# Performance work log

Hardware: AMD Instinct MI355X
Metric: run time of the kernel (lower is better)

Reference implementation:

```python
import jax, jax.numpy as jnp
import numpy as np

NUM_EMBEDDINGS = 512
EMBEDDING_DIM = 64
COMMITMENT_COST = 0.25


def setup_inputs() -> dict:
    key = jax.random.key(0)
    k1, k2 = jax.random.split(key)
    z_e = jax.random.normal(k1, (16, EMBEDDING_DIM, 64, 64), dtype=jnp.float32)
    # embedding.weight initialized uniform(-1/K, 1/K) in the torch module
    lim = 1.0 / NUM_EMBEDDINGS
    embedding = jax.random.uniform(
        k2, (NUM_EMBEDDINGS, EMBEDDING_DIM), dtype=jnp.float32,
        minval=-lim, maxval=lim)
    return {"z_e": z_e, "embedding": embedding}


def reference(z_e, embedding):
    b, c, h, w = z_e.shape
    K = embedding.shape[0]
    # NCHW -> NHWC -> [N, D]
    flat = jnp.transpose(z_e, (0, 2, 3, 1)).reshape(-1, c)  # [N, D]
    distances = (jnp.sum(flat * flat, axis=1, keepdims=True)
                 + jnp.sum(embedding * embedding, axis=1)
                 - 2.0 * jnp.matmul(flat, embedding.T))
    encoding_indices = jnp.argmin(distances, axis=1)  # [N]
    # one_hot @ embedding == gather (same math, avoids materializing [N,K] fp mm)
    z_q_flat = jnp.take(embedding, encoding_indices, axis=0)  # [N, D]
    z_q = jnp.transpose(z_q_flat.reshape(b, h, w, c), (0, 3, 1, 2))  # NCHW
    # EMA codebook: only commitment loss, codes updated via EMA (detached)
    e_latent_loss = jnp.mean((jax.lax.stop_gradient(z_q) - z_e) ** 2)
    loss = COMMITMENT_COST * e_latent_loss
    # straight-through estimator
    z_q_st = z_e + jax.lax.stop_gradient(z_q - z_e)
    # perplexity from one-hot assignment frequencies
    counts = jnp.zeros((K,), dtype=jnp.float32).at[encoding_indices].add(1.0)
    avg_probs = counts / flat.shape[0]
    perplexity = jnp.exp(-jnp.sum(avg_probs * jnp.log(avg_probs + 1e-10)))
    return z_q_st, loss, perplexity, encoding_indices
```

## Files before the change

### kernel.cpp

```cpp
#include <hip/hip_runtime.h>

#define BATCH 16
#define CH 64
#define HW 4096
#define NPIX 65536
#define KCODES 512
#define DDIM 64
#define NELEM 4194304

#define OUT_LOSS 4194304
#define OUT_PPL  4194305
#define OUT_IDX  4194306

#define MARGIN 2.2e-4f

typedef short bf16x8 __attribute__((ext_vector_type(8)));
typedef float f32x4  __attribute__((ext_vector_type(4)));

__device__ __forceinline__ float rnd(float s) {
    asm volatile("" : "+v"(s));
    return s;
}
__device__ __forceinline__ short f2bf(float f) {
    unsigned u = __builtin_bit_cast(unsigned, f);
    unsigned r = (u + 0x7fffu + ((u >> 16) & 1u)) >> 16;
    return (short)r;
}

__global__ void k_prep(const float* __restrict__ emb, float* __restrict__ e2,
                       bf16x8* __restrict__ Bh, float4* __restrict__ P4) {
    int gid = blockIdx.x * 256 + threadIdx.x;
    if (gid < 4096) {
        int tn = gid >> 7, rem = gid & 127;
        int chunk = (rem >> 6) & 1, q = (rem >> 4) & 3, i = rem & 15;
        int code = tn * 16 + i;
        const float* src = emb + code * DDIM + chunk * 32 + q * 8;
        bf16x8 h;
        #pragma unroll
        for (int j = 0; j < 8; ++j) h[j] = f2bf(src[j]);
        Bh[gid] = h;
    } else if (gid < 4608) {
        int k = gid - 4096;
        const float* row = emb + k * DDIM;
        float r[8];
        #pragma unroll
        for (int j = 0; j < 8; ++j) { float v = row[j]; r[j] = rnd(v * v); }
        #pragma unroll
        for (int m = 1; m < 8; ++m)
            #pragma unroll
            for (int j = 0; j < 8; ++j) { float v = row[8 * m + j]; r[j] += rnd(v * v); }
        e2[k] = ((r[0] + r[1]) + (r[2] + r[3])) + ((r[4] + r[5]) + (r[6] + r[7]));
    } else if (gid < 12800) {
        int pid = gid - 4608;
        int kk = pid >> 10, c4 = (pid >> 6) & 15, lane = pid & 63;
        int code = lane * 8 + kk;
        P4[pid] = *(const float4*)(emb + code * DDIM + c4 * 4);
    }
}

#define ROWW 40
__global__ __launch_bounds__(256, 4) void k_dist(
        const float* __restrict__ z_e, const float* __restrict__ emb,
        const bf16x8* __restrict__ Bh, const float* __restrict__ e2g,
        int* __restrict__ idx, int* __restrict__ glist, int* __restrict__ nflag,
        int* __restrict__ counts, float* __restrict__ slots,
        float* __restrict__ out) {
    __shared__ unsigned AhU[64 * ROWW];
    __shared__ bf16x8 Bs[1024];
    __shared__ float e2s[512];
    __shared__ int   hist[512];
    __shared__ int   flist[64];
    __shared__ int   fcnt, fbase;

    int t = threadIdx.x;
    int pxbase = blockIdx.x * 64;
    int batch = pxbase >> 12;
    int p0 = pxbase & 4095;
    const float* zb = z_e + (size_t)batch * (CH * HW) + p0;

    hist[t] = 0; hist[t + 256] = 0;
    e2s[t] = e2g[t]; e2s[t + 256] = e2g[t + 256];
    if (t == 0) fcnt = 0;

    #pragma unroll
    for (int it = 0; it < 8; ++it) {
        int i = it * 256 + t;
        int cp = i >> 6;
        int pp = i & 63;
        float v0 = zb[(2 * cp) * HW + pp];
        float v1 = zb[(2 * cp + 1) * HW + pp];
        AhU[pp * ROWW + cp] = (unsigned)(unsigned short)f2bf(v0)
                            | ((unsigned)(unsigned short)f2bf(v1) << 16);
    }
    __syncthreads();

    int w = t >> 6, lane = t & 63, col = lane & 15, quad = lane >> 4;

    const short* Ahs = (const short*)AhU;
    int m = w * 16 + col;
    bf16x8 a0 = *(const bf16x8*)(Ahs + m * (2 * ROWW) + quad * 8);
    bf16x8 a1 = *(const bf16x8*)(Ahs + m * (2 * ROWW) + 32 + quad * 8);

    float m1[4], m2[4];
    int   i1[4];
    #pragma unroll
    for (int r = 0; r < 4; ++r) { m1[r] = 1e30f; m2[r] = 1e30f; i1[r] = 0; }

    for (int qtr = 0; qtr < 4; ++qtr) {
        __syncthreads();
        #pragma unroll
        for (int it = 0; it < 4; ++it) Bs[it * 256 + t] = Bh[qtr * 1024 + it * 256 + t];
        __syncthreads();
        #pragma unroll
        for (int tn8 = 0; tn8 < 8; ++tn8) {
            int tn = qtr * 8 + tn8;
            bf16x8 c0 = Bs[tn8 * 128 + lane];
            bf16x8 c1 = Bs[tn8 * 128 + 64 + lane];
            float e2v = e2s[tn * 16 + col];
            int n = tn * 16 + col;
            f32x4 acc = {0.f, 0.f, 0.f, 0.f};
            acc = __builtin_amdgcn_mfma_f32_16x16x32_bf16(a0, c0, acc, 0, 0, 0);
            acc = __builtin_amdgcn_mfma_f32_16x16x32_bf16(a1, c1, acc, 0, 0, 0);
            #pragma unroll
            for (int r = 0; r < 4; ++r) {
                float d = fmaf(-2.0f, acc[r], e2v);
                if (d < m1[r])      { m2[r] = m1[r]; m1[r] = d; i1[r] = n; }
                else if (d < m2[r]) { m2[r] = d; }
            }
        }
    }

    #pragma unroll
    for (int off = 1; off < 16; off <<= 1) {
        #pragma unroll
        for (int r = 0; r < 4; ++r) {
            float om1 = __shfl_xor(m1[r], off);
            float om2 = __shfl_xor(m2[r], off);
            int   oi  = __shfl_xor(i1[r], off);
            if (om1 < m1[r] || (om1 == m1[r] && oi < i1[r])) {
                m2[r] = fminf(m1[r], om2);
                m1[r] = om1;
                i1[r] = oi;
            } else {
                m2[r] = fminf(m2[r], om1);
            }
        }
    }

    if (col == 0) {
        #pragma unroll
        for (int r = 0; r < 4; ++r) {
            int g = pxbase + w * 16 + quad * 4 + r;
            idx[g] = i1[r];
            out[OUT_IDX + g] = (float)i1[r];
            atomicAdd(&hist[i1[r]], 1);
            if (m2[r] - m1[r] < MARGIN) {
                int pos = atomicAdd(&fcnt, 1);
                flist[pos] = g;
            }
        }
    }

    int q4 = lane & 3;
    int bidx[4];
    #pragma unroll
    for (int j = 0; j < 4; ++j) bidx[j] = __shfl(i1[j], q4 << 4);
    const float* zw = zb + w * 16;
    float* ow = out + (size_t)batch * (CH * HW) + p0 + w * 16;
    float lsum = 0.0f;
    #pragma unroll
    for (int it = 0; it < 4; ++it) {
        int c = it * 16 + (lane >> 2);
        float4 ze = *(const float4*)(zw + c * HW + q4 * 4);
        float d0 = emb[bidx[0] * DDIM + c] - ze.x;
        float d1 = emb[bidx[1] * DDIM + c] - ze.y;
        float d2 = emb[bidx[2] * DDIM + c] - ze.z;
        float d3 = emb[bidx[3] * DDIM + c] - ze.w;
        float4 o = {ze.x + d0, ze.y + d1, ze.z + d2, ze.w + d3};
        *(float4*)(ow + c * HW + q4 * 4) = o;
        lsum = lsum + d0 * d0 + d1 * d1 + d2 * d2 + d3 * d3;
    }
    #pragma unroll
    for (int off = 32; off; off >>= 1) lsum += __shfl_down(lsum, off);
    if (lane == 0) atomicAdd(&slots[((blockIdx.x * 4 + w) & 63) * 16], lsum);

    __syncthreads();
    int v0 = hist[t];       if (v0) atomicAdd(&counts[t], v0);
    int v1 = hist[t + 256]; if (v1) atomicAdd(&counts[t + 256], v1);
    if (t == 0) fbase = atomicAdd(nflag, fcnt);
    __syncthreads();
    if (t < fcnt) glist[fbase + t] = flist[t];
}

__global__ __launch_bounds__(256) void k_refine(
        const float* __restrict__ z_e, const float* __restrict__ emb,
        const float* __restrict__ e2, const float4* __restrict__ P4,
        const int* __restrict__ glist, const int* __restrict__ nflag,
        int* __restrict__ idx, int* __restrict__ counts,
        float* __restrict__ slots, float* __restrict__ out) {
    __shared__ float4 Ps[2048];
    __shared__ float  xs[32][64];

    int t = threadIdx.x;
    int w = t >> 6, lane = t & 63;
    int wid = blockIdx.x * 4 + w;
    int n = nflag[0];
    if (blockIdx.x * 4 >= n) return;

    float4 ea = ((const float4*)e2)[lane * 2];
    float4 eb = ((const float4*)e2)[lane * 2 + 1];
    float e2v[8] = {ea.x, ea.y, ea.z, ea.w, eb.x, eb.y, eb.z, eb.w};

    for (int s = 0; s * 8192 + blockIdx.x * 4 < n; ++s) {
        int gidx[8];
        int nf = 0;
        #pragma unroll
        for (int f = 0; f < 8; ++f) {
            int j = s * 8192 + f * 1024 + wid;
            if (j < n) {
                int g = glist[j];
                gidx[nf] = g;
                int b = g >> 12, p = g & 4095;
                xs[w * 8 + nf][lane] = z_e[(size_t)b * (CH * HW) + (size_t)lane * HW + p];
                ++nf;
            }
        }
        __threadfence_block();

        float x2f[8];
        for (int f = 0; f < nf; ++f) {
            const float* xr = xs[w * 8 + f];
            float r[8];
            #pragma unroll
            for (int j = 0; j < 8; ++j) { float v = xr[j]; r[j] = rnd(v * v); }
            #pragma unroll
            for (int mm = 1; mm < 8; ++mm)
                #pragma unroll
                for (int j = 0; j < 8; ++j) { float v = xr[8 * mm + j]; r[j] += rnd(v * v); }
            x2f[f] = ((r[0] + r[1]) + (r[2] + r[3])) + ((r[4] + r[5]) + (r[6] + r[7]));
        }

        float bestd[8];
        int   besti[8];
        #pragma unroll
        for (int f = 0; f < 8; ++f) { bestd[f] = INFINITY; besti[f] = 1 << 30; }

        for (int qtr = 0; qtr < 4; ++qtr) {
            __syncthreads();
            #pragma unroll
            for (int it = 0; it < 8; ++it) Ps[it * 256 + t] = P4[qtr * 2048 + it * 256 + t];
            __syncthreads();
            for (int f = 0; f < nf; ++f) {
                const float* xr = xs[w * 8 + f];
                #pragma unroll
                for (int kk2 = 0; kk2 < 2; ++kk2) {
                    double d0 = 0.0, d1 = 0.0, d2 = 0.0, d3 = 0.0;
                    #pragma unroll
                    for (int c4 = 0; c4 < 16; ++c4) {
                        float4 xq = *(const float4*)&xr[c4 * 4];
                        float4 ev = Ps[(kk2 * 16 + c4) * 64 + lane];
                        d0 = fma((double)xq.x, (double)ev.x, d0);
                        d1 = fma((double)xq.y, (double)ev.y, d1);
                        d2 = fma((double)xq.z, (double)ev.z, d2);
                        d3 = fma((double)xq.w, (double)ev.w, d3);
                    }
                    int kk = qtr * 2 + kk2;
                    float dotf = (float)((d0 + d1) + (d2 + d3));
                    float tt = x2f[f] + e2v[kk];
                    float d = tt - 2.0f * dotf;
                    if (d < bestd[f]) { bestd[f] = d; besti[f] = lane * 8 + kk; }
                }
            }
        }

        for (int f = 0; f < nf; ++f) {
            float bd = bestd[f];
            int   bi = besti[f];
            #pragma unroll
            for (int off = 32; off; off >>= 1) {
                float od = __shfl_down(bd, off);
                int   oi = __shfl_down(bi, off);
                if (od < bd || (od == bd && oi < bi)) { bd = od; bi = oi; }
            }
            bi = __shfl(bi, 0);
            int g = gidx[f];
            int old = idx[g];
            if (bi != old) {
                int b = g >> 12, p = g & 4095;
                float xc = xs[w * 8 + f][lane];
                float qn = emb[bi * DDIM + lane];
                float qo = emb[old * DDIM + lane];
                float dn = qn - xc, dold = qo - xc;
                out[(size_t)b * (CH * HW) + (size_t)lane * HW + p] = xc + dn;
                float delta = dn * dn - dold * dold;
                #pragma unroll
                for (int off = 32; off; off >>= 1) delta += __shfl_down(delta, off);
                if (lane == 0) {
                    atomicAdd(&slots[(wid & 63) * 16], delta);
                    atomicAdd(&counts[old], -1);
                    atomicAdd(&counts[bi], 1);
                    idx[g] = bi;
                    out[OUT_IDX + g] = (float)bi;
                }
            }
        }
    }
}

__global__ void k_final(const int* __restrict__ counts,
                        const float* __restrict__ slots,
                        float* __restrict__ out) {
    int t = threadIdx.x;
    float cnt = (float)counts[t];
    float pb = cnt * (1.0f / 65536.0f);
    float term = pb * logf(pb + 1e-10f);
    #pragma unroll
    for (int off = 32; off; off >>= 1) term += __shfl_down(term, off);
    __shared__ float ls[8];
    __shared__ float lsum;
    int lane = t & 63, w = t >> 6;
    if (lane == 0) ls[w] = term;
    if (w == 0) {
        float s2 = slots[lane * 16];
        #pragma unroll
        for (int off = 32; off; off >>= 1) s2 += __shfl_down(s2, off);
        if (lane == 0) lsum = s2;
    }
    __syncthreads();
    if (t == 0) {
        float s = 0.0f;
        #pragma unroll
        for (int i = 0; i < 8; ++i) s += ls[i];
        out[OUT_PPL]  = expf(-s);
        out[OUT_LOSS] = 0.25f * (lsum / (float)NELEM);
    }
}

extern "C" void kernel_launch(void* const* d_in, const int* in_sizes, int n_in,
                              void* d_out, int out_size, void* d_ws, size_t ws_size,
                              hipStream_t stream) {
    const float* z_e = (const float*)d_in[0];
    const float* emb = (const float*)d_in[1];
    float* out = (float*)d_out;
    char* ws = (char*)d_ws;

    int*    idx    = (int*)(ws);
    int*    glist  = (int*)(ws + 262144);
    float*  e2     = (float*)(ws + 524288);
    int*    nflag  = (int*)(ws + 526336);
    int*    counts = (int*)(ws + 526400);
    float*  slots  = (float*)(ws + 528448);
    bf16x8* Bh     = (bf16x8*)(ws + 532544);
    float4* P4     = (float4*)(ws + 598080);

    hipMemsetAsync(ws + 526336, 0, 532544 - 526336, stream);

    k_prep<<<50, 256, 0, stream>>>(emb, e2, Bh, P4);
    k_dist<<<NPIX / 64, 256, 0, stream>>>(z_e, emb, Bh, e2, idx, glist, nflag, counts, slots, out);
    k_refine<<<256, 256, 0, stream>>>(z_e, emb, e2, P4, glist, nflag, idx, counts, slots, out);
    k_final<<<1, 512, 0, stream>>>(counts, slots, out);
}
```

Measured before the change: 150.1 us.

## Load full codebook into LDS once, widen dist blocks, simplify refine loop

The distance kernel now uses 512-thread blocks covering 128 pixels. It loads the whole bf16 codebook (64KB) into shared memory once instead of in four synchronised quarters, and builds the A fragments directly from global memory, dropping the transposed LDS staging. The refine kernel loads the full fp32 codebook panel (128KB LDS) once per block and processes one flagged pixel per wave per iteration, removing the repeated quarter reloads and barriers. The large LDS footprints reduce occupancy, and the direct strided global reads for A may be less coalesced.

```diff
diff --git a/kernel.cpp b/kernel.cpp
--- a/kernel.cpp
+++ b/kernel.cpp
@@ -58,75 +58,65 @@
     }
 }
 
-#define ROWW 40
-__global__ __launch_bounds__(256, 4) void k_dist(
+__global__ __launch_bounds__(512, 4) void k_dist(
         const float* __restrict__ z_e, const float* __restrict__ emb,
         const bf16x8* __restrict__ Bh, const float* __restrict__ e2g,
         int* __restrict__ idx, int* __restrict__ glist, int* __restrict__ nflag,
         int* __restrict__ counts, float* __restrict__ slots,
         float* __restrict__ out) {
-    __shared__ unsigned AhU[64 * ROWW];
-    __shared__ bf16x8 Bs[1024];
+    __shared__ bf16x8 Bs[4096];
     __shared__ float e2s[512];
     __shared__ int   hist[512];
-    __shared__ int   flist[64];
+    __shared__ int   flist[128];
     __shared__ int   fcnt, fbase;
 
     int t = threadIdx.x;
-    int pxbase = blockIdx.x * 64;
+    int pxbase = blockIdx.x * 128;
     int batch = pxbase >> 12;
     int p0 = pxbase & 4095;
     const float* zb = z_e + (size_t)batch * (CH * HW) + p0;
 
-    hist[t] = 0; hist[t + 256] = 0;
-    e2s[t] = e2g[t]; e2s[t + 256] = e2g[t + 256];
+    bf16x8 rb[8];
+    #pragma unroll
+    for (int i = 0; i < 8; ++i) rb[i] = Bh[i * 512 + t];
+
+    hist[t] = 0;
+    e2s[t] = e2g[t];
     if (t == 0) fcnt = 0;
 
-    #pragma unroll
-    for (int it = 0; it < 8; ++it) {
-        int i = it * 256 + t;
-        int cp = i >> 6;
-        int pp = i & 63;
-        float v0 = zb[(2 * cp) * HW + pp];
-        float v1 = zb[(2 * cp + 1) * HW + pp];
-        AhU[pp * ROWW + cp] = (unsigned)(unsigned short)f2bf(v0)
-                            | ((unsigned)(unsigned short)f2bf(v1) << 16);
-    }
-    __syncthreads();
-
     int w = t >> 6, lane = t & 63, col = lane & 15, quad = lane >> 4;
-
-    const short* Ahs = (const short*)AhU;
-    int m = w * 16 + col;
-    bf16x8 a0 = *(const bf16x8*)(Ahs + m * (2 * ROWW) + quad * 8);
-    bf16x8 a1 = *(const bf16x8*)(Ahs + m * (2 * ROWW) + 32 + quad * 8);
+    int px = w * 16 + col;
+
+    bf16x8 a0, a1;
+    #pragma unroll
+    for (int j = 0; j < 8; ++j) {
+        a0[j] = f2bf(zb[(quad * 8 + j) * HW + px]);
+        a1[j] = f2bf(zb[(32 + quad * 8 + j) * HW + px]);
+    }
+
+    #pragma unroll
+    for (int i = 0; i < 8; ++i) Bs[i * 512 + t] = rb[i];
+    __syncthreads();
 
     float m1[4], m2[4];
     int   i1[4];
     #pragma unroll
     for (int r = 0; r < 4; ++r) { m1[r] = 1e30f; m2[r] = 1e30f; i1[r] = 0; }
 
-    for (int qtr = 0; qtr < 4; ++qtr) {
-        __syncthreads();
-        #pragma unroll
-        for (int it = 0; it < 4; ++it) Bs[it * 256 + t] = Bh[qtr * 1024 + it * 256 + t];
-        __syncthreads();
-        #pragma unroll
-        for (int tn8 = 0; tn8 < 8; ++tn8) {
-            int tn = qtr * 8 + tn8;
-            bf16x8 c0 = Bs[tn8 * 128 + lane];
-            bf16x8 c1 = Bs[tn8 * 128 + 64 + lane];
-            float e2v = e2s[tn * 16 + col];
-            int n = tn * 16 + col;
-            f32x4 acc = {0.f, 0.f, 0.f, 0.f};
-            acc = __builtin_amdgcn_mfma_f32_16x16x32_bf16(a0, c0, acc, 0, 0, 0);
-            acc = __builtin_amdgcn_mfma_f32_16x16x32_bf16(a1, c1, acc, 0, 0, 0);
-            #pragma unroll
-            for (int r = 0; r < 4; ++r) {
-                float d = fmaf(-2.0f, acc[r], e2v);
-                if (d < m1[r])      { m2[r] = m1[r]; m1[r] = d; i1[r] = n; }
-                else if (d < m2[r]) { m2[r] = d; }
-            }
+    #pragma unroll 4
+    for (int tn = 0; tn < 32; ++tn) {
+        bf16x8 c0 = Bs[tn * 128 + lane];
+        bf16x8 c1 = Bs[tn * 128 + 64 + lane];
+        float e2v = e2s[tn * 16 + col];
+        int n = tn * 16 + col;
+        f32x4 acc = {0.f, 0.f, 0.f, 0.f};
+        acc = __builtin_amdgcn_mfma_f32_16x16x32_bf16(a0, c0, acc, 0, 0, 0);
+        acc = __builtin_amdgcn_mfma_f32_16x16x32_bf16(a1, c1, acc, 0, 0, 0);
+        #pragma unroll
+        for (int r = 0; r < 4; ++r) {
+            float d = fmaf(-2.0f, acc[r], e2v);
+            if (d < m1[r])      { m2[r] = m1[r]; m1[r] = d; i1[r] = n; }
+            else if (d < m2[r]) { m2[r] = d; }
         }
     }
 
@@ -182,11 +172,11 @@
     }
     #pragma unroll
     for (int off = 32; off; off >>= 1) lsum += __shfl_down(lsum, off);
-    if (lane == 0) atomicAdd(&slots[((blockIdx.x * 4 + w) & 63) * 16], lsum);
-
-    __syncthreads();
-    int v0 = hist[t];       if (v0) atomicAdd(&counts[t], v0);
-    int v1 = hist[t + 256]; if (v1) atomicAdd(&counts[t + 256], v1);
+    if (lane == 0) atomicAdd(&slots[((blockIdx.x * 8 + w) & 63) * 16], lsum);
+
+    __syncthreads();
+    int v0 = hist[t];
+    if (v0) atomicAdd(&counts[t], v0);
     if (t == 0) fbase = atomicAdd(nflag, fcnt);
     __syncthreads();
     if (t < fcnt) glist[fbase + t] = flist[t];
@@ -198,110 +188,82 @@
         const int* __restrict__ glist, const int* __restrict__ nflag,
         int* __restrict__ idx, int* __restrict__ counts,
         float* __restrict__ slots, float* __restrict__ out) {
-    __shared__ float4 Ps[2048];
-    __shared__ float  xs[32][64];
+    __shared__ float4 Ps[8192];
+    __shared__ float  xs[4][64];
 
     int t = threadIdx.x;
     int w = t >> 6, lane = t & 63;
-    int wid = blockIdx.x * 4 + w;
     int n = nflag[0];
-    if (blockIdx.x * 4 >= n) return;
+    if (blockIdx.x >= n) return;
+
+    #pragma unroll
+    for (int i = 0; i < 32; ++i) Ps[i * 256 + t] = P4[i * 256 + t];
+    __syncthreads();
 
     float4 ea = ((const float4*)e2)[lane * 2];
     float4 eb = ((const float4*)e2)[lane * 2 + 1];
     float e2v[8] = {ea.x, ea.y, ea.z, ea.w, eb.x, eb.y, eb.z, eb.w};
 
-    for (int s = 0; s * 8192 + blockIdx.x * 4 < n; ++s) {
-        int gidx[8];
-        int nf = 0;
-        #pragma unroll
-        for (int f = 0; f < 8; ++f) {
-            int j = s * 8192 + f * 1024 + wid;
-            if (j < n) {
-                int g = glist[j];
-                gidx[nf] = g;
-                int b = g >> 12, p = g & 4095;
-                xs[w * 8 + nf][lane] = z_e[(size_t)b * (CH * HW) + (size_t)lane * HW + p];
-                ++nf;
+    int wid = blockIdx.x * 4 + w;
+    for (int j = wid; j < n; j += 1024) {
+        int g = glist[j];
+        int b = g >> 12, p = g & 4095;
+        xs[w][lane] = z_e[(size_t)b * (CH * HW) + (size_t)lane * HW + p];
+        __threadfence_block();
+
+        const float* xr = xs[w];
+        float r[8];
+        #pragma unroll
+        for (int jj = 0; jj < 8; ++jj) { float v = xr[jj]; r[jj] = rnd(v * v); }
+        #pragma unroll
+        for (int mm = 1; mm < 8; ++mm)
+            #pragma unroll
+            for (int jj = 0; jj < 8; ++jj) { float v = xr[8 * mm + jj]; r[jj] += rnd(v * v); }
+        float x2 = ((r[0] + r[1]) + (r[2] + r[3])) + ((r[4] + r[5]) + (r[6] + r[7]));
+
+        float bestd = INFINITY;
+        int besti = 1 << 30;
+        #pragma unroll
+        for (int kk = 0; kk < 8; ++kk) {
+            double d0 = 0.0, d1 = 0.0, d2 = 0.0, d3 = 0.0;
+            #pragma unroll
+            for (int c4 = 0; c4 < 16; ++c4) {
+                float4 xq = *(const float4*)&xr[c4 * 4];
+                float4 ev = Ps[(kk * 16 + c4) * 64 + lane];
+                d0 = fma((double)xq.x, (double)ev.x, d0);
+                d1 = fma((double)xq.y, (double)ev.y, d1);
+                d2 = fma((double)xq.z, (double)ev.z, d2);
+                d3 = fma((double)xq.w, (double)ev.w, d3);
             }
-        }
-        __threadfence_block();
-
-        float x2f[8];
-        for (int f = 0; f < nf; ++f) {
-            const float* xr = xs[w * 8 + f];
-            float r[8];
+            float dotf = (float)((d0 + d1) + (d2 + d3));
+            float tt = x2 + e2v[kk];
+            float d = tt - 2.0f * dotf;
+            if (d < bestd) { bestd = d; besti = lane * 8 + kk; }
+        }
+        #pragma unroll
+        for (int off = 32; off; off >>= 1) {
+            float od = __shfl_down(bestd, off);
+            int   oi = __shfl_down(besti, off);
+            if (od < bestd || (od == bestd && oi < besti)) { bestd = od; besti = oi; }
+        }
+        besti = __shfl(besti, 0);
+
+        int old = idx[g];
+        if (besti != old) {
+            float xc = xr[lane];
+            float qn = emb[besti * DDIM + lane];
+            float qo = emb[old * DDIM + lane];
+            float dn = qn - xc, dold = qo - xc;
+            out[(size_t)b * (CH * HW) + (size_t)lane * HW + p] = xc + dn;
+            float delta = dn * dn - dold * dold;
             #pragma unroll
-            for (int j = 0; j < 8; ++j) { float v = xr[j]; r[j] = rnd(v * v); }
-            #pragma unroll
-            for (int mm = 1; mm < 8; ++mm)
-                #pragma unroll
-                for (int j = 0; j < 8; ++j) { float v = xr[8 * mm + j]; r[j] += rnd(v * v); }
-            x2f[f] = ((r[0] + r[1]) + (r[2] + r[3])) + ((r[4] + r[5]) + (r[6] + r[7]));
-        }
-
-        float bestd[8];
-        int   besti[8];
-        #pragma unroll
-        for (int f = 0; f < 8; ++f) { bestd[f] = INFINITY; besti[f] = 1 << 30; }
-
-        for (int qtr = 0; qtr < 4; ++qtr) {
-            __syncthreads();
-            #pragma unroll
-            for (int it = 0; it < 8; ++it) Ps[it * 256 + t] = P4[qtr * 2048 + it * 256 + t];
-            __syncthreads();
-            for (int f = 0; f < nf; ++f) {
-                const float* xr = xs[w * 8 + f];
-                #pragma unroll
-                for (int kk2 = 0; kk2 < 2; ++kk2) {
-                    double d0 = 0.0, d1 = 0.0, d2 = 0.0, d3 = 0.0;
-                    #pragma unroll
-                    for (int c4 = 0; c4 < 16; ++c4) {
-                        float4 xq = *(const float4*)&xr[c4 * 4];
-                        float4 ev = Ps[(kk2 * 16 + c4) * 64 + lane];
-                        d0 = fma((double)xq.x, (double)ev.x, d0);
-                        d1 = fma((double)xq.y, (double)ev.y, d1);
-                        d2 = fma((double)xq.z, (double)ev.z, d2);
-                        d3 = fma((double)xq.w, (double)ev.w, d3);
-                    }
-                    int kk = qtr * 2 + kk2;
-                    float dotf = (float)((d0 + d1) + (d2 + d3));
-                    float tt = x2f[f] + e2v[kk];
-                    float d = tt - 2.0f * dotf;
-                    if (d < bestd[f]) { bestd[f] = d; besti[f] = lane * 8 + kk; }
-                }
-            }
-        }
-
-        for (int f = 0; f < nf; ++f) {
-            float bd = bestd[f];
-            int   bi = besti[f];
-            #pragma unroll
-            for (int off = 32; off; off >>= 1) {
-                float od = __shfl_down(bd, off);
-                int   oi = __shfl_down(bi, off);
-                if (od < bd || (od == bd && oi < bi)) { bd = od; bi = oi; }
-            }
-            bi = __shfl(bi, 0);
-            int g = gidx[f];
-            int old = idx[g];
-            if (bi != old) {
-                int b = g >> 12, p = g & 4095;
-                float xc = xs[w * 8 + f][lane];
-                float qn = emb[bi * DDIM + lane];
-                float qo = emb[old * DDIM + lane];
-                float dn = qn - xc, dold = qo - xc;
-                out[(size_t)b * (CH * HW) + (size_t)lane * HW + p] = xc + dn;
-                float delta = dn * dn - dold * dold;
-                #pragma unroll
-                for (int off = 32; off; off >>= 1) delta += __shfl_down(delta, off);
-                if (lane == 0) {
-                    atomicAdd(&slots[(wid & 63) * 16], delta);
-                    atomicAdd(&counts[old], -1);
-                    atomicAdd(&counts[bi], 1);
-                    idx[g] = bi;
-                    out[OUT_IDX + g] = (float)bi;
-                }
+            for (int off = 32; off; off >>= 1) delta += __shfl_down(delta, off);
+            if (lane == 0) {
+                atomicAdd(&slots[(wid & 63) * 16], delta);
+                atomicAdd(&counts[old], -1);
+                atomicAdd(&counts[besti], 1);
+                idx[g] = besti;
+                out[OUT_IDX + g] = (float)besti;
             }
         }
     }
@@ -356,7 +318,7 @@
     hipMemsetAsync(ws + 526336, 0, 532544 - 526336, stream);
 
     k_prep<<<50, 256, 0, stream>>>(emb, e2, Bh, P4);
-    k_dist<<<NPIX / 64, 256, 0, stream>>>(z_e, emb, Bh, e2, idx, glist, nflag, counts, slots, out);
+    k_dist<<<NPIX / 128, 512, 0, stream>>>(z_e, emb, Bh, e2, idx, glist, nflag, counts, slots, out);
     k_refine<<<256, 256, 0, stream>>>(z_e, emb, e2, P4, glist, nflag, idx, counts, slots, out);
     k_final<<<1, 512, 0, stream>>>(counts, slots, out);
 }
```

New measurement: 139.6 us. 1.08x faster.
